# Optimization experiments

Hardware: AMD Instinct MI355X
Metric: run time of the kernel (lower is better)

The kernel has to match this reference:

```python
import jax, jax.numpy as jnp
import numpy as np

HEAD_SIZE = 8
QK_DIM = 512
V_DIM = 512
N = 4096
ATT_DIM = QK_DIM // HEAD_SIZE  # 64
SCALE = ATT_DIM ** (-0.5)
NEG_FILL = jnp.float32(-9e15)


def setup_inputs() -> dict:
    key = jax.random.key(0)
    k1, k2, k3, k4 = jax.random.split(key, 4)
    x1 = jax.random.normal(k1, (N, QK_DIM), dtype=jnp.float32)
    x2 = jax.random.normal(k2, (N, QK_DIM), dtype=jnp.float32)
    v = jax.random.normal(k3, (N, V_DIM), dtype=jnp.float32)
    adj = jax.random.randint(k4, (N, N), 0, 2, dtype=jnp.int32)
    return {"x1": x1, "x2": x2, "v": v, "adj": adj}


def reference(x1, x2, v, adj):
    n = x1.shape[0]
    # [N, H, d] -> [H, N, d]
    q = x1.reshape(n, HEAD_SIZE, -1).transpose(1, 0, 2) * SCALE
    k = x2.reshape(n, HEAD_SIZE, -1).transpose(1, 0, 2)
    vv = v.reshape(n, HEAD_SIZE, -1).transpose(1, 0, 2)
    # [H, N, N] dense scores, masked by adjacency (broadcast over heads)
    scores = jnp.einsum('hnd,hmd->hnm', q, k)
    scores = jnp.where(adj > 0, scores, NEG_FILL)
    attn = jax.nn.softmax(scores, axis=-1)
    out = jnp.einsum('hnm,hmd->hnd', attn, vv)
    # [H, N, d] -> [N, H*d]
    return out.transpose(1, 0, 2).reshape(n, -1)
```

## Files before the change

kernel.cpp:

```cpp
#include <hip/hip_runtime.h>

#define NN 4096
#define HEADS 8
#define DD 64
#define QKD 512

typedef __attribute__((ext_vector_type(8))) short short8;
typedef __attribute__((ext_vector_type(4))) float f32x4;
typedef __attribute__((ext_vector_type(4))) float float4v;
typedef __attribute__((ext_vector_type(4))) int int4v;
typedef unsigned int u32;
typedef unsigned short u16;
typedef unsigned long long u64;

union U8 { u16 u[8]; short8 s; };
union U4 { u32 u[4]; short8 s; };

__device__ __forceinline__ u16 f2bf(float f) {
  u32 u = __float_as_uint(f);
  u += 0x7fffu + ((u >> 16) & 1u);
  return (u16)(u >> 16);
}

#define GLL(src, dst) __builtin_amdgcn_global_load_lds( \
    (const __attribute__((address_space(1))) void*)(src), \
    (__attribute__((address_space(3))) void*)(dst), 16, 0, 0)

__global__ __launch_bounds__(256) void prepass_fused(
    const float* __restrict__ x2, const float* __restrict__ v,
    const int* __restrict__ adj,
    u16* __restrict__ Kbt, u16* __restrict__ Vbt, u64* __restrict__ Abg)
{
  __shared__ u16 Vtmp[64][80];
  const int b = blockIdx.x;
  const int t = threadIdx.x;

  if (b < 4096) {
    const int row = b;
    const int w = t >> 6, lane = t & 63;
    const int* base = adj + (size_t)row * NN;
    #pragma unroll
    for (int i = 0; i < 16; i++) {
      int idx = w * 16 + i;
      int val = base[idx * 64 + lane];
      u64 m = __ballot(val > 0);
      if (lane == 0) Abg[(size_t)row * 64 + idx] = m;
    }
  } else if (b < 4608) {
    const int j = b - 4096;
    const int h = j >> 6, kb = j & 63;
    u16* dst = Kbt + (size_t)j * 4096;
    #pragma unroll
    for (int i = 0; i < 2; i++) {
      int c = t + i * 256;
      int off = c * 16;
      int kr = off >> 7;
      int db = (off & 127) ^ ((kr & 7) << 4);
      int d0 = db >> 1;
      const float* p = x2 + (size_t)(kb * 64 + kr) * QKD + h * DD + d0;
      float4v a0 = *(const float4v*)p;
      float4v a1 = *(const float4v*)(p + 4);
      U8 r;
      r.u[0] = f2bf(a0.x); r.u[1] = f2bf(a0.y); r.u[2] = f2bf(a0.z); r.u[3] = f2bf(a0.w);
      r.u[4] = f2bf(a1.x); r.u[5] = f2bf(a1.y); r.u[6] = f2bf(a1.z); r.u[7] = f2bf(a1.w);
      *(short8*)((char*)dst + off) = r.s;
    }
  } else {
    const int bb = b - 4608;
    const int h = bb >> 6, kb = bb & 63;
    {
      int k = t >> 2, j0 = (t & 3) * 16;
      const float* p = v + (size_t)(kb * 64 + k) * QKD + h * DD + j0;
      float4v a0 = *(const float4v*)p;
      float4v a1 = *(const float4v*)(p + 4);
      float4v a2 = *(const float4v*)(p + 8);
      float4v a3 = *(const float4v*)(p + 12);
      U8 r0, r1;
      r0.u[0] = f2bf(a0.x); r0.u[1] = f2bf(a0.y); r0.u[2] = f2bf(a0.z); r0.u[3] = f2bf(a0.w);
      r0.u[4] = f2bf(a1.x); r0.u[5] = f2bf(a1.y); r0.u[6] = f2bf(a1.z); r0.u[7] = f2bf(a1.w);
      r1.u[0] = f2bf(a2.x); r1.u[1] = f2bf(a2.y); r1.u[2] = f2bf(a2.z); r1.u[3] = f2bf(a2.w);
      r1.u[4] = f2bf(a3.x); r1.u[5] = f2bf(a3.y); r1.u[6] = f2bf(a3.z); r1.u[7] = f2bf(a3.w);
      *(short8*)(&Vtmp[k][j0]) = r0.s;
      *(short8*)(&Vtmp[k][j0 + 8]) = r1.s;
    }
    __syncthreads();
    u16* dst = Vbt + (size_t)bb * 4096;
    #pragma unroll
    for (int i = 0; i < 2; i++) {
      int c = t + i * 256;
      int off = c * 16;
      int vd = off >> 7;
      int kbyte = (off & 127) ^ ((vd & 7) << 4);
      int k0 = kbyte >> 1;
      U8 r;
      #pragma unroll
      for (int jj = 0; jj < 8; jj++) r.u[jj] = Vtmp[k0 + jj][vd];
      *(short8*)((char*)dst + off) = r.s;
    }
  }
}

__global__ __launch_bounds__(256) void attn_fast(
    const float* __restrict__ x1,
    const u64* __restrict__ Abg,
    const u16* __restrict__ Kbt, const u16* __restrict__ Vbt,
    float* __restrict__ out)
{
  __shared__ u16 Klds[2][4096];
  __shared__ u16 Vlds[2][4096];

  const int b = blockIdx.x;
  const int widx = ((b & 7) << 6) | (b >> 3);
  const int qt = widx >> 3;
  const int h = widx & 7;
  const int t = threadIdx.x;
  const int w = t >> 6;
  const int lane = t & 63;
  const int g = lane >> 4;
  const int qi = lane & 15;
  const int qrow = qt * 64 + w * 16 + qi;

  const u16* Ktiles = Kbt + (size_t)h * 64 * 4096;
  const u16* Vtiles = Vbt + (size_t)h * 64 * 4096;
  const u64* arow = Abg + (size_t)qrow * 64;

  const float SCL = 0.125f * 1.4426950408889634f;
  short8 qfrag[2];
  #pragma unroll
  for (int dc = 0; dc < 2; dc++) {
    const float* p = x1 + (size_t)qrow * QKD + h * DD + dc * 32 + g * 8;
    float4v a = *(const float4v*)p;
    float4v c = *(const float4v*)(p + 4);
    U8 r;
    r.u[0] = f2bf(a.x * SCL); r.u[1] = f2bf(a.y * SCL);
    r.u[2] = f2bf(a.z * SCL); r.u[3] = f2bf(a.w * SCL);
    r.u[4] = f2bf(c.x * SCL); r.u[5] = f2bf(c.y * SCL);
    r.u[6] = f2bf(c.z * SCL); r.u[7] = f2bf(c.w * SCL);
    qfrag[dc] = r.s;
  }

  const f32x4 zero = {0.f, 0.f, 0.f, 0.f};
  f32x4 Ot[4] = {zero, zero, zero, zero};
  float mrun = -1e30f;
  float lsum = 0.f;

  {
    const u16* sk = Ktiles + t * 8;
    const u16* sv = Vtiles + t * 8;
    u16* dk = &Klds[0][t * 8];
    u16* dv = &Vlds[0][t * 8];
    GLL(sk, dk);
    GLL(sk + 2048, dk + 2048);
    GLL(sv, dv);
    GLL(sv + 2048, dv + 2048);
  }
  u64 adjcur = arow[0];
  __syncthreads();

  int cur = 0;
  for (int kb = 0; kb < NN / 64; kb++) {
    u64 adjnext = 0;
    if (kb < NN / 64 - 1) {
      const u16* sk = Ktiles + (size_t)(kb + 1) * 4096 + t * 8;
      const u16* sv = Vtiles + (size_t)(kb + 1) * 4096 + t * 8;
      u16* dk = &Klds[cur ^ 1][t * 8];
      u16* dv = &Vlds[cur ^ 1][t * 8];
      GLL(sk, dk);
      GLL(sk + 2048, dk + 2048);
      GLL(sv, dv);
      GLL(sv + 2048, dv + 2048);
      adjnext = arow[kb + 1];
    }

    const char* kbase = (const char*)Klds[cur];
    f32x4 st[4] = {zero, zero, zero, zero};
    #pragma unroll
    for (int tk = 0; tk < 4; tk++) {
      int krow = tk * 16 + qi;
      #pragma unroll
      for (int dc = 0; dc < 2; dc++) {
        int off = (krow * 128 + (dc * 32 + g * 8) * 2) ^ ((krow & 7) << 4);
        short8 af = *(const short8*)(kbase + off);
        st[tk] = __builtin_amdgcn_mfma_f32_16x16x32_bf16(af, qfrag[dc], st[tk], 0, 0, 0);
      }
    }

    u32 blo = (u32)adjcur, bhi = (u32)(adjcur >> 32);

    float tmax = -1e30f;
    #pragma unroll
    for (int tk = 0; tk < 4; tk++) {
      u32 half = (tk < 2) ? blo : bhi;
      int bb0 = (tk & 1) * 16 + g * 4;
      #pragma unroll
      for (int r = 0; r < 4; r++) {
        float s = st[tk][r];
        s = ((half >> (bb0 + r)) & 1u) ? s : -9e15f;
        st[tk][r] = s;
        tmax = fmaxf(tmax, s);
      }
    }
    tmax = fmaxf(tmax, __shfl_xor(tmax, 16));
    tmax = fmaxf(tmax, __shfl_xor(tmax, 32));
    float newm = fmaxf(mrun, tmax);
    float alpha = __builtin_amdgcn_exp2f(mrun - newm);
    mrun = newm;

    float psum = 0.f;
    u32 pk[8];
    #pragma unroll
    for (int tk = 0; tk < 4; tk++) {
      float p0 = __builtin_amdgcn_exp2f(st[tk][0] - newm);
      float p1 = __builtin_amdgcn_exp2f(st[tk][1] - newm);
      float p2 = __builtin_amdgcn_exp2f(st[tk][2] - newm);
      float p3 = __builtin_amdgcn_exp2f(st[tk][3] - newm);
      psum += (p0 + p1) + (p2 + p3);
      pk[tk * 2 + 0] = (u32)f2bf(p0) | ((u32)f2bf(p1) << 16);
      pk[tk * 2 + 1] = (u32)f2bf(p2) | ((u32)f2bf(p3) << 16);
    }
    psum += __shfl_xor(psum, 16);
    psum += __shfl_xor(psum, 32);
    lsum = lsum * alpha + psum;
    #pragma unroll
    for (int tv = 0; tv < 4; tv++) {
      Ot[tv][0] *= alpha; Ot[tv][1] *= alpha; Ot[tv][2] *= alpha; Ot[tv][3] *= alpha;
    }

    const char* vbase = (const char*)Vlds[cur];
    const int srcbase = qi + ((g & 1) << 5);
    #pragma unroll
    for (int kc = 0; kc < 2; kc++) {
      U4 pf;
      #pragma unroll
      for (int jp = 0; jp < 4; jp++) {
        int src = srcbase + ((jp >> 1) << 4);
        u32 va1 = (u32)__shfl((int)pk[4 * kc + (jp & 1)], src);
        u32 vb1 = (u32)__shfl((int)pk[4 * kc + 2 + (jp & 1)], src);
        pf.u[jp] = (g < 2) ? va1 : vb1;
      }
      #pragma unroll
      for (int tv = 0; tv < 4; tv++) {
        int vd = tv * 16 + qi;
        int off = (vd * 128 + (kc * 32 + g * 8) * 2) ^ ((vd & 7) << 4);
        short8 vfrag = *(const short8*)(vbase + off);
        Ot[tv] = __builtin_amdgcn_mfma_f32_16x16x32_bf16(vfrag, pf.s, Ot[tv], 0, 0, 0);
      }
    }

    __syncthreads();
    adjcur = adjnext;
    cur ^= 1;
  }

  float inv = 1.0f / lsum;
  #pragma unroll
  for (int tv = 0; tv < 4; tv++) {
    float4v o;
    o.x = Ot[tv][0] * inv; o.y = Ot[tv][1] * inv;
    o.z = Ot[tv][2] * inv; o.w = Ot[tv][3] * inv;
    *(float4v*)(out + (size_t)qrow * QKD + h * DD + tv * 16 + g * 4) = o;
  }
}

__global__ __launch_bounds__(512) void attn_fallback(
    const float* __restrict__ x1, const float* __restrict__ x2f,
    const float* __restrict__ vf, const int* __restrict__ adj,
    float* __restrict__ out)
{
  __shared__ u16 Klds[64 * 128];
  __shared__ u16 Vlds[128 * 64];
  __shared__ u64 Abits[64];

  const int b = blockIdx.x;
  const int qt = (b & 7) | ((b >> 5) << 3);
  const int hg = (b >> 3) & 3;
  const int h0 = hg * 2;
  const int t = threadIdx.x;
  const int w = t >> 6;
  const int lane = t & 63;
  const int qsub = w >> 1;
  const int hh = w & 1;
  const int h = h0 + hh;
  const int g = lane >> 4;
  const int qi = lane & 15;
  const int qbase = qt * 64;
  const int q_local = qsub * 16 + qi;
  const int qrow = qbase + q_local;

  const float SCL = 0.125f * 1.4426950408889634f;
  short8 qfrag[2];
  #pragma unroll
  for (int dc = 0; dc < 2; dc++) {
    const float* p = x1 + (size_t)qrow * QKD + h * DD + dc * 32 + g * 8;
    float4v a = *(const float4v*)p;
    float4v c = *(const float4v*)(p + 4);
    U8 r;
    r.u[0] = f2bf(a.x * SCL); r.u[1] = f2bf(a.y * SCL);
    r.u[2] = f2bf(a.z * SCL); r.u[3] = f2bf(a.w * SCL);
    r.u[4] = f2bf(c.x * SCL); r.u[5] = f2bf(c.y * SCL);
    r.u[6] = f2bf(c.z * SCL); r.u[7] = f2bf(c.w * SCL);
    qfrag[dc] = r.s;
  }

  const f32x4 zero = {0.f, 0.f, 0.f, 0.f};
  f32x4 Ot[4] = {zero, zero, zero, zero};
  float mrun = -1e30f;
  float lsum = 0.f;

  for (int kb = 0; kb < NN / 64; kb++) {
    const int k0 = kb * 64;
    __syncthreads();
    #pragma unroll
    for (int i = 0; i < 2; i++) {
      int s = t + i * 512;
      int row = s >> 4, c0 = (s & 15) * 8;
      int off = (row * 256 + c0 * 2) ^ ((row & 7) << 4);
      const float* p = x2f + (size_t)(k0 + row) * QKD + h0 * DD + c0;
      float4v a = *(const float4v*)p;
      float4v c = *(const float4v*)(p + 4);
      U8 r;
      r.u[0]=f2bf(a.x); r.u[1]=f2bf(a.y); r.u[2]=f2bf(a.z); r.u[3]=f2bf(a.w);
      r.u[4]=f2bf(c.x); r.u[5]=f2bf(c.y); r.u[6]=f2bf(c.z); r.u[7]=f2bf(c.w);
      *(short8*)((char*)Klds + off) = r.s;
    }
    {
      int vdg = t & 15, kp = t >> 4;
      int vd0 = vdg * 8, kk = kp * 2;
      u16 ua[8], ub[8];
      const float* pa = vf + (size_t)(k0 + kk) * QKD + h0 * DD + vd0;
      float4v a0 = *(const float4v*)pa;
      float4v a1 = *(const float4v*)(pa + 4);
      float4v b0 = *(const float4v*)(pa + QKD);
      float4v b1 = *(const float4v*)(pa + QKD + 4);
      ua[0]=f2bf(a0.x); ua[1]=f2bf(a0.y); ua[2]=f2bf(a0.z); ua[3]=f2bf(a0.w);
      ua[4]=f2bf(a1.x); ua[5]=f2bf(a1.y); ua[6]=f2bf(a1.z); ua[7]=f2bf(a1.w);
      ub[0]=f2bf(b0.x); ub[1]=f2bf(b0.y); ub[2]=f2bf(b0.z); ub[3]=f2bf(b0.w);
      ub[4]=f2bf(b1.x); ub[5]=f2bf(b1.y); ub[6]=f2bf(b1.z); ub[7]=f2bf(b1.w);
      #pragma unroll
      for (int j = 0; j < 8; j++) {
        u32 pk2 = (u32)ua[j] | ((u32)ub[j] << 16);
        int vd = vd0 + j;
        int off = (vd * 128 + kk * 2) ^ (((vd & 7) ^ ((vd >> 3) & 7)) << 4);
        *(u32*)((char*)Vlds + off) = pk2;
      }
    }
    {
      int row = t >> 3, c8 = t & 7;
      const int* ap = adj + (size_t)(qbase + row) * NN + k0 + c8 * 8;
      int4v a0 = *(const int4v*)ap;
      int4v a1 = *(const int4v*)(ap + 4);
      u32 byteval = (u32)(a0.x > 0)        | ((u32)(a0.y > 0) << 1) |
                    ((u32)(a0.z > 0) << 2) | ((u32)(a0.w > 0) << 3) |
                    ((u32)(a1.x > 0) << 4) | ((u32)(a1.y > 0) << 5) |
                    ((u32)(a1.z > 0) << 6) | ((u32)(a1.w > 0) << 7);
      ((unsigned char*)Abits)[row * 8 + c8] = (unsigned char)byteval;
    }
    __syncthreads();

    f32x4 st[4] = {zero, zero, zero, zero};
    #pragma unroll
    for (int tk = 0; tk < 4; tk++) {
      #pragma unroll
      for (int dc = 0; dc < 2; dc++) {
        int krow = tk * 16 + qi;
        int c = hh * 64 + dc * 32 + g * 8;
        int off = (krow * 256 + c * 2) ^ ((krow & 7) << 4);
        short8 af = *(const short8*)((char*)Klds + off);
        st[tk] = __builtin_amdgcn_mfma_f32_16x16x32_bf16(af, qfrag[dc], st[tk], 0, 0, 0);
      }
    }

    u64 bbm = Abits[q_local];
    u32 blo = (u32)bbm, bhi = (u32)(bbm >> 32);

    float tmax = -1e30f;
    #pragma unroll
    for (int tk = 0; tk < 4; tk++) {
      u32 half = (tk < 2) ? blo : bhi;
      int bb0 = (tk & 1) * 16 + g * 4;
      #pragma unroll
      for (int r = 0; r < 4; r++) {
        float s = st[tk][r];
        s = ((half >> (bb0 + r)) & 1u) ? s : -9e15f;
        st[tk][r] = s;
        tmax = fmaxf(tmax, s);
      }
    }
    tmax = fmaxf(tmax, __shfl_xor(tmax, 16));
    tmax = fmaxf(tmax, __shfl_xor(tmax, 32));
    float newm = fmaxf(mrun, tmax);
    float alpha = __builtin_amdgcn_exp2f(mrun - newm);
    mrun = newm;

    float psum = 0.f;
    u32 pk[8];
    #pragma unroll
    for (int tk = 0; tk < 4; tk++) {
      float p0 = __builtin_amdgcn_exp2f(st[tk][0] - newm);
      float p1 = __builtin_amdgcn_exp2f(st[tk][1] - newm);
      float p2 = __builtin_amdgcn_exp2f(st[tk][2] - newm);
      float p3 = __builtin_amdgcn_exp2f(st[tk][3] - newm);
      psum += (p0 + p1) + (p2 + p3);
      pk[tk * 2 + 0] = (u32)f2bf(p0) | ((u32)f2bf(p1) << 16);
      pk[tk * 2 + 1] = (u32)f2bf(p2) | ((u32)f2bf(p3) << 16);
    }
    psum += __shfl_xor(psum, 16);
    psum += __shfl_xor(psum, 32);
    lsum = lsum * alpha + psum;
    #pragma unroll
    for (int tv = 0; tv < 4; tv++) {
      Ot[tv][0] *= alpha; Ot[tv][1] *= alpha; Ot[tv][2] *= alpha; Ot[tv][3] *= alpha;
    }

    const int srcbase = qi + ((g & 1) << 5);
    #pragma unroll
    for (int kc = 0; kc < 2; kc++) {
      U4 pf;
      #pragma unroll
      for (int jp = 0; jp < 4; jp++) {
        int src = srcbase + ((jp >> 1) << 4);
        u32 va1 = (u32)__shfl((int)pk[4 * kc + (jp & 1)], src);
        u32 vb1 = (u32)__shfl((int)pk[4 * kc + 2 + (jp & 1)], src);
        pf.u[jp] = (g < 2) ? va1 : vb1;
      }
      #pragma unroll
      for (int tv = 0; tv < 4; tv++) {
        int vd = hh * 64 + tv * 16 + qi;
        int off = (vd * 128 + (kc * 32 + g * 8) * 2) ^ (((vd & 7) ^ ((vd >> 3) & 7)) << 4);
        short8 vfrag = *(const short8*)((char*)Vlds + off);
        Ot[tv] = __builtin_amdgcn_mfma_f32_16x16x32_bf16(vfrag, pf.s, Ot[tv], 0, 0, 0);
      }
    }
  }

  float inv = 1.0f / lsum;
  #pragma unroll
  for (int tv = 0; tv < 4; tv++) {
    float4v o;
    o.x = Ot[tv][0] * inv; o.y = Ot[tv][1] * inv;
    o.z = Ot[tv][2] * inv; o.w = Ot[tv][3] * inv;
    *(float4v*)(out + (size_t)qrow * QKD + h * DD + tv * 16 + g * 4) = o;
  }
}

extern "C" void kernel_launch(void* const* d_in, const int* in_sizes, int n_in,
                              void* d_out, int out_size, void* d_ws, size_t ws_size,
                              hipStream_t stream) {
  const float* x1 = (const float*)d_in[0];
  const float* x2 = (const float*)d_in[1];
  const float* v  = (const float*)d_in[2];
  const int* adj  = (const int*)d_in[3];
  float* out = (float*)d_out;

  const size_t szK = (size_t)512 * 4096 * sizeof(u16);
  const size_t szV = szK;
  const size_t szA = (size_t)NN * 64 * sizeof(u64);
  const size_t need = szK + szV + szA;

  if (ws_size >= need && d_ws != nullptr) {
    u16* Kbt = (u16*)d_ws;
    u16* Vbt = (u16*)((char*)d_ws + szK);
    u64* Abg = (u64*)((char*)d_ws + szK + szV);
    prepass_fused<<<dim3(5120), dim3(256), 0, stream>>>(x2, v, adj, Kbt, Vbt, Abg);
    attn_fast<<<dim3(512), dim3(256), 0, stream>>>(x1, Abg, Kbt, Vbt, out);
  } else {
    attn_fallback<<<dim3(256), dim3(512), 0, stream>>>(x1, x2, v, adj, out);
  }
}
```

Baseline: 224.6 us.

## Vectorize adjacency bitpacking, skip unneeded rescale, use hardware bf16 pack, set MFMA priority

The adjacency prepass now loads 16 ints per thread with vector loads and packs them into bits through shared memory, replacing the per-wave ballot loop. The attention loop skips the running-max rescale of the output accumulators when no lane's max increased. It converts P to bf16 with a single v_cvt_pk_bf16_f32 instruction instead of manual rounding. It also raises wave priority around the MFMA blocks. These cut VALU work in the softmax section and prepass memory overhead, but they add a wave-uniform branch and rely on the packed-convert instruction rounding the same way.

```diff
diff --git a/kernel.cpp b/kernel.cpp
--- a/kernel.cpp
+++ b/kernel.cpp
@@ -20,6 +20,12 @@
   u32 u = __float_as_uint(f);
   u += 0x7fffu + ((u >> 16) & 1u);
   return (u16)(u >> 16);
+}
+
+__device__ __forceinline__ u32 cvtpk(float lo, float hi) {
+  u32 d;
+  asm("v_cvt_pk_bf16_f32 %0, %1, %2" : "=v"(d) : "v"(lo), "v"(hi));
+  return d;
 }
 
 #define GLL(src, dst) __builtin_amdgcn_global_load_lds( \
@@ -37,14 +43,26 @@
 
   if (b < 4096) {
     const int row = b;
-    const int w = t >> 6, lane = t & 63;
-    const int* base = adj + (size_t)row * NN;
-    #pragma unroll
-    for (int i = 0; i < 16; i++) {
-      int idx = w * 16 + i;
-      int val = base[idx * 64 + lane];
-      u64 m = __ballot(val > 0);
-      if (lane == 0) Abg[(size_t)row * 64 + idx] = m;
+    const int* src = adj + (size_t)row * NN;
+    int4v a0 = *(const int4v*)(src + t * 16);
+    int4v a1 = *(const int4v*)(src + t * 16 + 4);
+    int4v a2 = *(const int4v*)(src + t * 16 + 8);
+    int4v a3 = *(const int4v*)(src + t * 16 + 12);
+    u32 bits =
+        (u32)(a0.x > 0)         | ((u32)(a0.y > 0) << 1)  |
+        ((u32)(a0.z > 0) << 2)  | ((u32)(a0.w > 0) << 3)  |
+        ((u32)(a1.x > 0) << 4)  | ((u32)(a1.y > 0) << 5)  |
+        ((u32)(a1.z > 0) << 6)  | ((u32)(a1.w > 0) << 7)  |
+        ((u32)(a2.x > 0) << 8)  | ((u32)(a2.y > 0) << 9)  |
+        ((u32)(a2.z > 0) << 10) | ((u32)(a2.w > 0) << 11) |
+        ((u32)(a3.x > 0) << 12) | ((u32)(a3.y > 0) << 13) |
+        ((u32)(a3.z > 0) << 14) | ((u32)(a3.w > 0) << 15);
+    unsigned char* AB = (unsigned char*)Vtmp;
+    *(u16*)(AB + t * 2) = (u16)bits;
+    __syncthreads();
+    if (t < 64) {
+      u64 m = *(const u64*)(AB + t * 8);
+      Abg[(size_t)row * 64 + t] = m;
     }
   } else if (b < 4608) {
     const int j = b - 4096;
@@ -174,6 +192,7 @@
 
     const char* kbase = (const char*)Klds[cur];
     f32x4 st[4] = {zero, zero, zero, zero};
+    __builtin_amdgcn_s_setprio(1);
     #pragma unroll
     for (int tk = 0; tk < 4; tk++) {
       int krow = tk * 16 + qi;
@@ -184,10 +203,10 @@
         st[tk] = __builtin_amdgcn_mfma_f32_16x16x32_bf16(af, qfrag[dc], st[tk], 0, 0, 0);
       }
     }
+    __builtin_amdgcn_s_setprio(0);
 
     u32 blo = (u32)adjcur, bhi = (u32)(adjcur >> 32);
 
-    float tmax = -1e30f;
     #pragma unroll
     for (int tk = 0; tk < 4; tk++) {
       u32 half = (tk < 2) ? blo : bhi;
@@ -195,36 +214,43 @@
       #pragma unroll
       for (int r = 0; r < 4; r++) {
         float s = st[tk][r];
-        s = ((half >> (bb0 + r)) & 1u) ? s : -9e15f;
-        st[tk][r] = s;
-        tmax = fmaxf(tmax, s);
-      }
-    }
+        st[tk][r] = ((half >> (bb0 + r)) & 1u) ? s : -9e15f;
+      }
+    }
+    float t0 = fmaxf(fmaxf(st[0][0], st[0][1]), fmaxf(st[0][2], st[0][3]));
+    float t1 = fmaxf(fmaxf(st[1][0], st[1][1]), fmaxf(st[1][2], st[1][3]));
+    float t2 = fmaxf(fmaxf(st[2][0], st[2][1]), fmaxf(st[2][2], st[2][3]));
+    float t3 = fmaxf(fmaxf(st[3][0], st[3][1]), fmaxf(st[3][2], st[3][3]));
+    float tmax = fmaxf(fmaxf(t0, t1), fmaxf(t2, t3));
     tmax = fmaxf(tmax, __shfl_xor(tmax, 16));
     tmax = fmaxf(tmax, __shfl_xor(tmax, 32));
-    float newm = fmaxf(mrun, tmax);
-    float alpha = __builtin_amdgcn_exp2f(mrun - newm);
-    mrun = newm;
+
+    if (!__all(tmax <= mrun)) {
+      const float newm = fmaxf(mrun, tmax);
+      const float alpha = __builtin_amdgcn_exp2f(mrun - newm);
+      lsum *= alpha;
+      #pragma unroll
+      for (int tv = 0; tv < 4; tv++) {
+        Ot[tv][0] *= alpha; Ot[tv][1] *= alpha; Ot[tv][2] *= alpha; Ot[tv][3] *= alpha;
+      }
+      mrun = newm;
+    }
 
     float psum = 0.f;
     u32 pk[8];
     #pragma unroll
     for (int tk = 0; tk < 4; tk++) {
-      float p0 = __builtin_amdgcn_exp2f(st[tk][0] - newm);
-      float p1 = __builtin_amdgcn_exp2f(st[tk][1] - newm);
-      float p2 = __builtin_amdgcn_exp2f(st[tk][2] - newm);
-      float p3 = __builtin_amdgcn_exp2f(st[tk][3] - newm);
+      float p0 = __builtin_amdgcn_exp2f(st[tk][0] - mrun);
+      float p1 = __builtin_amdgcn_exp2f(st[tk][1] - mrun);
+      float p2 = __builtin_amdgcn_exp2f(st[tk][2] - mrun);
+      float p3 = __builtin_amdgcn_exp2f(st[tk][3] - mrun);
       psum += (p0 + p1) + (p2 + p3);
-      pk[tk * 2 + 0] = (u32)f2bf(p0) | ((u32)f2bf(p1) << 16);
-      pk[tk * 2 + 1] = (u32)f2bf(p2) | ((u32)f2bf(p3) << 16);
+      pk[tk * 2 + 0] = cvtpk(p0, p1);
+      pk[tk * 2 + 1] = cvtpk(p2, p3);
     }
     psum += __shfl_xor(psum, 16);
     psum += __shfl_xor(psum, 32);
-    lsum = lsum * alpha + psum;
-    #pragma unroll
-    for (int tv = 0; tv < 4; tv++) {
-      Ot[tv][0] *= alpha; Ot[tv][1] *= alpha; Ot[tv][2] *= alpha; Ot[tv][3] *= alpha;
-    }
+    lsum += psum;
 
     const char* vbase = (const char*)Vlds[cur];
     const int srcbase = qi + ((g & 1) << 5);
@@ -238,6 +264,7 @@
         u32 vb1 = (u32)__shfl((int)pk[4 * kc + 2 + (jp & 1)], src);
         pf.u[jp] = (g < 2) ? va1 : vb1;
       }
+      __builtin_amdgcn_s_setprio(1);
       #pragma unroll
       for (int tv = 0; tv < 4; tv++) {
         int vd = tv * 16 + qi;
@@ -245,6 +272,7 @@
         short8 vfrag = *(const short8*)(vbase + off);
         Ot[tv] = __builtin_amdgcn_mfma_f32_16x16x32_bf16(vfrag, pf.s, Ot[tv], 0, 0, 0);
       }
+      __builtin_amdgcn_s_setprio(0);
     }
 
     __syncthreads();
```

Result: faster. 209.5 us (-6.7%).
